# Performance work log

Hardware: AMD Instinct MI355X
Metric: run time of the kernel (lower is better)

Reference implementation:

```python
import jax, jax.numpy as jnp
import numpy as np

B, S, H, NH = 8, 1024, 1024, 16
HD = H // NH  # 64


def _rope(x, cos, sin):
    # x: [B, NH, S, HD]; cos/sin: [1, 1, S, HD]
    x1, x2 = jnp.split(x, 2, axis=-1)
    x_rot = jnp.concatenate((-x2, x1), axis=-1)
    return x * cos + x_rot * sin


def setup_inputs() -> dict:
    key = jax.random.key(0)
    ks = jax.random.split(key, 12)
    std = 1.0 / np.sqrt(H)
    inp = {
        "hidden_states": jax.random.normal(ks[0], (B, S, H), dtype=jnp.float32),
        "cos": jax.random.uniform(ks[1], (S, HD), dtype=jnp.float32),
        "sin": jax.random.uniform(ks[2], (S, HD), dtype=jnp.float32),
        "Wq": jax.random.normal(ks[3], (H, H), dtype=jnp.float32) * std,
        "bq": jnp.zeros((H,), dtype=jnp.float32),
        "Wk": jax.random.normal(ks[4], (H, H), dtype=jnp.float32) * std,
        "bk": jnp.zeros((H,), dtype=jnp.float32),
        "Wv": jax.random.normal(ks[5], (H, H), dtype=jnp.float32) * std,
        "bv": jnp.zeros((H,), dtype=jnp.float32),
        "Wo": jax.random.normal(ks[6], (H, H), dtype=jnp.float32) * std,
        "bo": jnp.zeros((H,), dtype=jnp.float32),
    }
    return inp


def reference(hidden_states, cos, sin, Wq, bq, Wk, bk, Wv, bv, Wo, bo):
    def split_heads(t):  # [B,S,H] -> [B,NH,S,HD]
        return t.reshape(B, S, NH, HD).transpose(0, 2, 1, 3)

    q = split_heads(hidden_states @ Wq.T + bq)
    k = split_heads(hidden_states @ Wk.T + bk)
    v = split_heads(hidden_states @ Wv.T + bv)

    c = cos.reshape(1, 1, S, HD)
    s = sin.reshape(1, 1, S, HD)
    q = _rope(q, c, s)
    k = _rope(k, c, s)

    scale = 1.0 / jnp.sqrt(jnp.asarray(HD, dtype=q.dtype))
    scores = jnp.einsum("bhqd,bhkd->bhqk", q, k) * scale
    attn = jax.nn.softmax(scores, axis=-1)
    out = jnp.einsum("bhqk,bhkd->bhqd", attn, v)  # [B,NH,S,HD]
    out = out.transpose(0, 2, 1, 3).reshape(B, S, H)
    return out @ Wo.T + bo
```

## Files before the change

kernel.cpp:

```cpp
#include <hip/hip_runtime.h>
#include <hip/hip_bf16.h>
#include <stdint.h>


typedef __bf16 bf16_t;
typedef __bf16 bf16x8 __attribute__((ext_vector_type(8)));
typedef __bf16 bf16x4 __attribute__((ext_vector_type(4)));
typedef float  f32x4  __attribute__((ext_vector_type(4)));
typedef float  f32x16 __attribute__((ext_vector_type(16)));
typedef uint32_t u32x4 __attribute__((ext_vector_type(4)));
typedef uint32_t u32x2 __attribute__((ext_vector_type(2)));

typedef __attribute__((address_space(1))) const void* as1_cvp;
typedef __attribute__((address_space(3))) void* as3_vp;

__device__ __forceinline__ f32x4 mfma16(bf16x8 a, bf16x8 b, f32x4 c) {
  return __builtin_amdgcn_mfma_f32_16x16x32_bf16(a, b, c, 0, 0, 0);
}
__device__ __forceinline__ f32x16 mfma32(bf16x8 a, bf16x8 b, f32x16 c) {
  return __builtin_amdgcn_mfma_f32_32x32x16_bf16(a, b, c, 0, 0, 0);
}

__device__ __forceinline__ void gload_lds16(const bf16_t* g, bf16_t* l) {
  __builtin_amdgcn_global_load_lds((as1_cvp)g, (as3_vp)l, 16, 0, 0);
}

__device__ __forceinline__ f32x4 zero4() {
  f32x4 z = {0.f, 0.f, 0.f, 0.f};
  return z;
}

__device__ __forceinline__ uint32_t pk2(float a, float b) {
  union { bf16_t h[2]; uint32_t u; } x;
  x.h[0] = (bf16_t)a;
  x.h[1] = (bf16_t)b;
  return x.u;
}

__global__ void cvt_all(const float* __restrict__ hs, const float* __restrict__ wq,
                        const float* __restrict__ wk, const float* __restrict__ wv,
                        const float* __restrict__ wo, bf16_t* __restrict__ Xb,
                        bf16_t* __restrict__ Wqkvb, bf16_t* __restrict__ Wob) {
  const int i = blockIdx.x * 256 + threadIdx.x;
  const f32x4* src;
  bf16x4* dst;
  if (i < 2097152) {
    src = (const f32x4*)hs + i;            dst = (bf16x4*)Xb + i;
  } else if (i < 2359296) {
    src = (const f32x4*)wq + (i - 2097152); dst = (bf16x4*)Wqkvb + (i - 2097152);
  } else if (i < 2621440) {
    src = (const f32x4*)wk + (i - 2359296); dst = (bf16x4*)Wqkvb + (i - 2359296) + 262144;
  } else if (i < 2883584) {
    src = (const f32x4*)wv + (i - 2621440); dst = (bf16x4*)Wqkvb + (i - 2621440) + 524288;
  } else {
    src = (const f32x4*)wo + (i - 2883584); dst = (bf16x4*)Wob + (i - 2883584);
  }
  const f32x4 v = *src;
  bf16x4 o;
  o[0] = (bf16_t)v[0]; o[1] = (bf16_t)v[1];
  o[2] = (bf16_t)v[2]; o[3] = (bf16_t)v[3];
  *dst = o;
}

template <int MODE>
__global__ __launch_bounds__(256, 3) void gemm128(
    const bf16_t* __restrict__ A, const bf16_t* __restrict__ Bw,
    const float* __restrict__ bQ, const float* __restrict__ bK,
    const float* __restrict__ bV, const float* __restrict__ cosp,
    const float* __restrict__ sinp,
    bf16_t* __restrict__ Qb, bf16_t* __restrict__ Kb, bf16_t* __restrict__ Vtb,
    float* __restrict__ Cout) {
  __shared__ bf16_t sm[128 * 64 * 2];
  bf16_t* sA = sm;
  bf16_t* sB = sm + 128 * 64;

  const int tid = threadIdx.x;
  const int lane = tid & 63;
  const int wid = tid >> 6;
  const int l15 = lane & 15;
  const int l4 = lane >> 4;
  const int row0 = blockIdx.x * 128;
  const int col0 = blockIdx.y * 128;
  const int wr = (wid >> 1) * 64;
  const int wc = (wid & 1) * 64;

  f32x4 acc[4][4];
#pragma unroll
  for (int mi = 0; mi < 4; ++mi)
#pragma unroll
    for (int ni = 0; ni < 4; ++ni) acc[mi][ni] = zero4();

  for (int kt = 0; kt < 16; ++kt) {
    const int k0 = kt * 64;
#pragma unroll
    for (int i = 0; i < 4; ++i) {
      const int chunk = i * 256 + tid;
      const int r = chunk >> 3, cc = chunk & 7;
      const int scc = cc ^ (r & 7);
      gload_lds16(A + (size_t)(row0 + r) * 1024 + k0 + scc * 8,
                  sA + (i * 256 + wid * 64) * 8);
      gload_lds16(Bw + (size_t)(col0 + r) * 1024 + k0 + scc * 8,
                  sB + (i * 256 + wid * 64) * 8);
    }
    __syncthreads();
    __builtin_amdgcn_s_setprio(1);
#pragma unroll
    for (int ks = 0; ks < 2; ++ks) {
      bf16x8 af[4], bfv[4];
#pragma unroll
      for (int mi = 0; mi < 4; ++mi) {
        const int r = wr + mi * 16 + l15;
        af[mi] = *(const bf16x8*)(sA + r * 64 + (((ks * 4 + l4) ^ (r & 7)) << 3));
      }
#pragma unroll
      for (int ni = 0; ni < 4; ++ni) {
        const int r = wc + ni * 16 + l15;
        bfv[ni] = *(const bf16x8*)(sB + r * 64 + (((ks * 4 + l4) ^ (r & 7)) << 3));
      }
#pragma unroll
      for (int mi = 0; mi < 4; ++mi)
#pragma unroll
        for (int ni = 0; ni < 4; ++ni)
          acc[mi][ni] = mfma16(af[mi], bfv[ni], acc[mi][ni]);
    }
    __builtin_amdgcn_s_setprio(0);
    __syncthreads();
  }

  if constexpr (MODE == 0) {
    const int proj = blockIdx.y >> 3;
    const float* bias = proj == 0 ? bQ : (proj == 1 ? bK : bV);
    if (proj < 2) {
      bf16_t* dst = proj == 0 ? Qb : Kb;
      const float qs = proj == 0 ? 0.18033688011112042f : 1.0f;
      const int base = col0 & 1023;
#pragma unroll
      for (int mi = 0; mi < 4; ++mi)
#pragma unroll
        for (int nl = 0; nl < 2; ++nl) {
          const int gcL = base + wc + nl * 16 + l15;
          const int h = gcL >> 6, dL = gcL & 63;
          const float bbL = bias[gcL], bbH = bias[gcL + 32];
#pragma unroll
          for (int j = 0; j < 4; ++j) {
            const int gr = row0 + wr + mi * 16 + l4 * 4 + j;
            const int b = gr >> 10, s = gr & 1023;
            const float cL = cosp[s * 64 + dL], cH = cosp[s * 64 + dL + 32];
            const float snL = sinp[s * 64 + dL], snH = sinp[s * 64 + dL + 32];
            const float x1 = acc[mi][nl][j] + bbL;
            const float x2 = acc[mi][nl + 2][j] + bbH;
            bf16_t* p = dst + ((size_t)(b * 16 + h) * 1024 + s) * 64 + dL;
            p[0]  = (bf16_t)((x1 * cL - x2 * snL) * qs);
            p[32] = (bf16_t)((x2 * cH + x1 * snH) * qs);
          }
        }
    } else {
      bf16_t* trb = sm;
#pragma unroll
      for (int mi = 0; mi < 4; ++mi)
#pragma unroll
        for (int ni = 0; ni < 4; ++ni) {
          const int cl = wc + ni * 16 + l15;
          const float bb = bias[(col0 & 1023) + cl];
#pragma unroll
          for (int j = 0; j < 4; ++j) {
            const int rl = wr + mi * 16 + l4 * 4 + j;
            trb[cl * 128 + (((rl >> 3) ^ (cl & 7)) << 3) + (rl & 7)] =
                (bf16_t)(acc[mi][ni][j] + bb);
          }
        }
      __syncthreads();
      const int b = row0 >> 10, s0 = row0 & 1023;
#pragma unroll
      for (int i = 0; i < 8; ++i) {
        const int chunk = i * 256 + tid;
        const int cl = chunk >> 4, rc = chunk & 15;
        const u32x4 v = *(const u32x4*)(trb + cl * 128 + ((rc ^ (cl & 7)) << 3));
        const int cv = (col0 & 1023) + cl;
        *(u32x4*)(Vtb + ((size_t)(b * 16 + (cv >> 6)) * 64 + (cv & 63)) * 1024 +
                  s0 + rc * 8) = v;
      }
    }
  } else {
#pragma unroll
    for (int mi = 0; mi < 4; ++mi)
#pragma unroll
      for (int ni = 0; ni < 4; ++ni) {
        const int gc = col0 + wc + ni * 16 + l15;
        const float bb = bQ[gc];
#pragma unroll
        for (int j = 0; j < 4; ++j) {
          const int gr = row0 + wr + mi * 16 + l4 * 4 + j;
          Cout[(size_t)gr * 1024 + gc] = acc[mi][ni][j] + bb;
        }
      }
  }
}

__global__ __launch_bounds__(256, 2) void attn_kernel(
    const bf16_t* __restrict__ Qb, const bf16_t* __restrict__ Kb,
    const bf16_t* __restrict__ Vtb, bf16_t* __restrict__ AOb) {
  __shared__ bf16_t sm[16384];
  bf16_t* sK = sm;
  bf16_t* sV = sm + 4096;
  const int tid = threadIdx.x, lane = tid & 63, wid = tid >> 6;
  const int l31 = lane & 31, l5 = lane >> 5;
  const bool loh = (l5 == 0);
  (void)loh;

  const int bh = blockIdx.x;
  const int q0 = blockIdx.y * 256;
  const bf16_t* Qg = Qb + (size_t)bh * 65536;
  const bf16_t* Kg = Kb + (size_t)bh * 65536;
  const bf16_t* Vg = Vtb + (size_t)bh * 65536;

#pragma unroll
  for (int i = 0; i < 8; ++i) {
    const int chunk = i * 256 + tid, r = chunk >> 3, c = chunk & 7;
    *(u32x4*)(sm + r * 64 + ((c ^ (r & 7)) << 3)) =
        *(const u32x4*)(Qg + (size_t)(q0 + r) * 64 + c * 8);
  }
  __syncthreads();
  bf16x8 qf[2][4];
#pragma unroll
  for (int qb = 0; qb < 2; ++qb)
#pragma unroll
    for (int step = 0; step < 4; ++step) {
      const int r = wid * 64 + qb * 32 + l31;
      qf[qb][step] =
          *(const bf16x8*)(sm + r * 64 + (((step * 2 + l5) ^ (r & 7)) << 3));
    }
  __syncthreads();

  const int ck1 = 256 + tid;
  const int kr0 = tid >> 3, kc0 = tid & 7;
  const int kr1 = ck1 >> 3, kc1 = ck1 & 7;
  bf16_t* kd0 = sK + kr0 * 64 + ((kc0 ^ (kr0 & 7)) << 3);
  bf16_t* kd1 = sK + kr1 * 64 + ((kc1 ^ (kr1 & 7)) << 3);
  bf16_t* vd0 = sV + kr0 * 64 + ((kc0 ^ (kr0 & 7)) << 3);
  bf16_t* vd1 = sV + kr1 * 64 + ((kc1 ^ (kr1 & 7)) << 3);
  const bf16_t* ksrc0 = Kg + kr0 * 64 + kc0 * 8;
  const bf16_t* ksrc1 = Kg + kr1 * 64 + kc1 * 8;
  const bf16_t* vsrc0 = Vg + kr0 * 1024 + kc0 * 8;
  const bf16_t* vsrc1 = Vg + kr1 * 1024 + kc1 * 8;

  u32x4 kv0 = *(const u32x4*)ksrc0;
  u32x4 kv1 = *(const u32x4*)ksrc1;
  u32x4 kv2 = *(const u32x4*)vsrc0;
  u32x4 kv3 = *(const u32x4*)vsrc1;

  f32x16 accO[2][2];
#pragma unroll
  for (int qb = 0; qb < 2; ++qb)
#pragma unroll
    for (int db = 0; db < 2; ++db)
#pragma unroll
      for (int r = 0; r < 16; ++r) accO[qb][db][r] = 0.f;
  float l_p[2] = {0.f, 0.f};

  for (int kt = 0; kt < 16; ++kt) {
    *(u32x4*)kd0 = kv0;
    *(u32x4*)kd1 = kv1;
    *(u32x4*)vd0 = kv2;
    *(u32x4*)vd1 = kv3;
    __syncthreads();
    if (kt < 15) {
      kv0 = *(const u32x4*)(ksrc0 + (kt + 1) * 4096);
      kv1 = *(const u32x4*)(ksrc1 + (kt + 1) * 4096);
      kv2 = *(const u32x4*)(vsrc0 + (kt + 1) * 64);
      kv3 = *(const u32x4*)(vsrc1 + (kt + 1) * 64);
    }

#pragma unroll
    for (int kb = 0; kb < 2; ++kb) {
      bf16x8 kf[4];
#pragma unroll
      for (int step = 0; step < 4; ++step) {
        const int r = kb * 32 + l31;
        kf[step] =
            *(const bf16x8*)(sK + r * 64 + (((step * 2 + l5) ^ (r & 7)) << 3));
      }
      f32x16 st0, st1;
#pragma unroll
      for (int r = 0; r < 16; ++r) { st0[r] = 0.f; st1[r] = 0.f; }
      __builtin_amdgcn_s_setprio(1);
#pragma unroll
      for (int step = 0; step < 4; ++step)
        st0 = mfma32(kf[step], qf[0][step], st0);
#pragma unroll
      for (int step = 0; step < 4; ++step)
        st1 = mfma32(kf[step], qf[1][step], st1);
      __builtin_amdgcn_s_setprio(0);

      float p0[16], p1[16];
      float rsa = 0.f, rsb = 0.f, rsc = 0.f, rsd = 0.f;
#pragma unroll
      for (int r = 0; r < 16; r += 2) {
        p0[r] = __builtin_amdgcn_exp2f(st0[r]);
        p0[r + 1] = __builtin_amdgcn_exp2f(st0[r + 1]);
        rsa += p0[r];
        rsb += p0[r + 1];
        p1[r] = __builtin_amdgcn_exp2f(st1[r]);
        p1[r + 1] = __builtin_amdgcn_exp2f(st1[r + 1]);
        rsc += p1[r];
        rsd += p1[r + 1];
      }
      l_p[0] += rsa + rsb;
      l_p[1] += rsc + rsd;

#pragma unroll
      for (int cb = 0; cb < 2; ++cb) {
        const int c = kb * 2 + cb;
        bf16x8 vf[2];
#pragma unroll
        for (int db = 0; db < 2; ++db) {
          const int d = db * 32 + l31;
          vf[db] =
              *(const bf16x8*)(sV + d * 64 + (((c * 2 + l5) ^ (d & 7)) << 3));
        }

        const uint32_t A0q0 = pk2(p0[8 * cb + 0], p0[8 * cb + 1]);
        const uint32_t B0q0 = pk2(p0[8 * cb + 2], p0[8 * cb + 3]);
        const uint32_t A1q0 = pk2(p0[8 * cb + 4], p0[8 * cb + 5]);
        const uint32_t B1q0 = pk2(p0[8 * cb + 6], p0[8 * cb + 7]);
        const uint32_t A0q1 = pk2(p1[8 * cb + 0], p1[8 * cb + 1]);
        const uint32_t B0q1 = pk2(p1[8 * cb + 2], p1[8 * cb + 3]);
        const uint32_t A1q1 = pk2(p1[8 * cb + 4], p1[8 * cb + 5]);
        const uint32_t B1q1 = pk2(p1[8 * cb + 6], p1[8 * cb + 7]);

        u32x4 w0, w1;
#if __has_builtin(__builtin_amdgcn_permlane32_swap)
        {
          const u32x2 ra0 = __builtin_amdgcn_permlane32_swap(A0q0, A1q0, false, false);
          const u32x2 rb0 = __builtin_amdgcn_permlane32_swap(B0q0, B1q0, false, false);
          w0[0] = ra0.x; w0[1] = rb0.x; w0[2] = ra0.y; w0[3] = rb0.y;
          const u32x2 ra1 = __builtin_amdgcn_permlane32_swap(A0q1, A1q1, false, false);
          const u32x2 rb1 = __builtin_amdgcn_permlane32_swap(B0q1, B1q1, false, false);
          w1[0] = ra1.x; w1[1] = rb1.x; w1[2] = ra1.y; w1[3] = rb1.y;
        }
#else
        {
          const uint32_t TAq0 = __shfl_xor(loh ? A1q0 : A0q0, 32);
          const uint32_t TBq0 = __shfl_xor(loh ? B1q0 : B0q0, 32);
          w0[0] = loh ? A0q0 : TAq0;
          w0[1] = loh ? B0q0 : TBq0;
          w0[2] = loh ? TAq0 : A1q0;
          w0[3] = loh ? TBq0 : B1q0;
          const uint32_t TAq1 = __shfl_xor(loh ? A1q1 : A0q1, 32);
          const uint32_t TBq1 = __shfl_xor(loh ? B1q1 : B0q1, 32);
          w1[0] = loh ? A0q1 : TAq1;
          w1[1] = loh ? B0q1 : TBq1;
          w1[2] = loh ? TAq1 : A1q1;
          w1[3] = loh ? TBq1 : B1q1;
        }
#endif
        const bf16x8 pa0 = __builtin_bit_cast(bf16x8, w0);
        const bf16x8 pa1 = __builtin_bit_cast(bf16x8, w1);

        __builtin_amdgcn_s_setprio(1);
        accO[0][0] = mfma32(vf[0], pa0, accO[0][0]);
        accO[0][1] = mfma32(vf[1], pa0, accO[0][1]);
        accO[1][0] = mfma32(vf[0], pa1, accO[1][0]);
        accO[1][1] = mfma32(vf[1], pa1, accO[1][1]);
        __builtin_amdgcn_s_setprio(0);
      }
    }
    __syncthreads();
  }

  float li[2];
#pragma unroll
  for (int qb = 0; qb < 2; ++qb) {
    const float t = l_p[qb] + __shfl_xor(l_p[qb], 32);
    li[qb] = __builtin_amdgcn_rcpf(t);
  }

  const int b = bh >> 4, h = bh & 15;
#pragma unroll
  for (int qb = 0; qb < 2; ++qb) {
    const int s = q0 + wid * 64 + qb * 32 + l31;
    bf16_t* rowp = AOb + ((size_t)b * 1024 + s) * 1024 + h * 64;
#pragma unroll
    for (int db = 0; db < 2; ++db)
#pragma unroll
      for (int g = 0; g < 4; ++g) {
        bf16x4 o;
#pragma unroll
        for (int j = 0; j < 4; ++j)
          o[j] = (bf16_t)(accO[qb][db][g * 4 + j] * li[qb]);
        *(bf16x4*)(rowp + db * 32 + g * 8 + l5 * 4) = o;
      }
  }
}

extern "C" void kernel_launch(void* const* d_in, const int* in_sizes, int n_in,
                              void* d_out, int out_size, void* d_ws,
                              size_t ws_size, hipStream_t stream) {
  const float* hs = (const float*)d_in[0];
  const float* cs = (const float*)d_in[1];
  const float* sn = (const float*)d_in[2];
  const float* Wq = (const float*)d_in[3];
  const float* bq = (const float*)d_in[4];
  const float* Wk = (const float*)d_in[5];
  const float* bk = (const float*)d_in[6];
  const float* Wv = (const float*)d_in[7];
  const float* bv = (const float*)d_in[8];
  const float* Wo = (const float*)d_in[9];
  const float* bo = (const float*)d_in[10];
  float* out = (float*)d_out;

  char* ws = (char*)d_ws;
  bf16_t* Xb    = (bf16_t*)(ws + 0);
  bf16_t* Wqkvb = (bf16_t*)(ws + 16777216);
  bf16_t* Wob   = (bf16_t*)(ws + 23068672);
  bf16_t* Qb    = (bf16_t*)(ws + 25165824);
  bf16_t* Kb    = (bf16_t*)(ws + 41943040);
  bf16_t* Vtb   = (bf16_t*)(ws + 58720256);
  bf16_t* AOb   = (bf16_t*)(ws + 75497472);

  cvt_all<<<12288, 256, 0, stream>>>(hs, Wq, Wk, Wv, Wo, Xb, Wqkvb, Wob);
  gemm128<0><<<dim3(64, 24), 256, 0, stream>>>(Xb, Wqkvb, bq, bk, bv, cs, sn,
                                               Qb, Kb, Vtb, nullptr);
  attn_kernel<<<dim3(128, 4), 256, 0, stream>>>(Qb, Kb, Vtb, AOb);
  gemm128<1><<<dim3(64, 8), 256, 0, stream>>>(AOb, Wob, bo, nullptr, nullptr,
                                              nullptr, nullptr, nullptr,
                                              nullptr, nullptr, out);
}
```

Before: 134.1 us.

## Double-buffer 128-key K/V tiles in LDS via direct global-to-LDS loads

Replaces the register-staged K/V prefetch (global load to registers, then LDS store, one 64-key tile per barrier) with global_load_lds direct copies into a double-buffered LDS region holding 128-key tiles. Q is also loaded straight into LDS. The aim is to halve the number of outer iterations and barriers, remove the VGPR staging, and overlap the next tile's load with compute. LDS use doubles to 64KB, which may limit occupancy at 2 blocks per CU. The visible part of the loop shows no barrier or waitcnt before the loads overwrite the alternate buffer, so correctness depends on code not shown.

After: 177.2 us. 32.2% more time.

```diff
diff --git a/kernel.cpp b/kernel.cpp
--- a/kernel.cpp
+++ b/kernel.cpp
@@ -200,9 +200,7 @@
 __global__ __launch_bounds__(256, 2) void attn_kernel(
     const bf16_t* __restrict__ Qb, const bf16_t* __restrict__ Kb,
     const bf16_t* __restrict__ Vtb, bf16_t* __restrict__ AOb) {
-  __shared__ bf16_t sm[16384];
-  bf16_t* sK = sm;
-  bf16_t* sV = sm + 4096;
+  __shared__ bf16_t sm[32768];
   const int tid = threadIdx.x, lane = tid & 63, wid = tid >> 6;
   const int l31 = lane & 31, l5 = lane >> 5;
   const bool loh = (l5 == 0);
@@ -214,13 +212,24 @@
   const bf16_t* Kg = Kb + (size_t)bh * 65536;
   const bf16_t* Vg = Vtb + (size_t)bh * 65536;
 
-#pragma unroll
-  for (int i = 0; i < 8; ++i) {
-    const int chunk = i * 256 + tid, r = chunk >> 3, c = chunk & 7;
-    *(u32x4*)(sm + r * 64 + ((c ^ (r & 7)) << 3)) =
-        *(const u32x4*)(Qg + (size_t)(q0 + r) * 64 + c * 8);
-  }
+  const int rr = tid >> 3, sc = (tid & 7) ^ (rr & 7);
+  const int dv = tid >> 4, sv = (tid & 15) ^ (dv & 7);
+  const bf16_t* Qsrc = Qg + (size_t)(q0 + rr) * 64 + sc * 8;
+  const bf16_t* Ksrc = Kg + (size_t)rr * 64 + sc * 8;
+  const bf16_t* Vsrc = Vg + (size_t)dv * 1024 + sv * 8;
+  const int dstw = wid * 512;
+
+#pragma unroll
+  for (int i = 0; i < 8; ++i)
+    gload_lds16(Qsrc + (size_t)i * 2048, sm + i * 2048 + dstw);
+#pragma unroll
+  for (int i = 0; i < 4; ++i)
+    gload_lds16(Ksrc + (size_t)i * 2048, sm + 16384 + i * 2048 + dstw);
+#pragma unroll
+  for (int i = 0; i < 4; ++i)
+    gload_lds16(Vsrc + (size_t)i * 16384, sm + 24576 + i * 2048 + dstw);
   __syncthreads();
+
   bf16x8 qf[2][4];
 #pragma unroll
   for (int qb = 0; qb < 2; ++qb)
@@ -232,23 +241,6 @@
     }
   __syncthreads();
 
-  const int ck1 = 256 + tid;
-  const int kr0 = tid >> 3, kc0 = tid & 7;
-  const int kr1 = ck1 >> 3, kc1 = ck1 & 7;
-  bf16_t* kd0 = sK + kr0 * 64 + ((kc0 ^ (kr0 & 7)) << 3);
-  bf16_t* kd1 = sK + kr1 * 64 + ((kc1 ^ (kr1 & 7)) << 3);
-  bf16_t* vd0 = sV + kr0 * 64 + ((kc0 ^ (kr0 & 7)) << 3);
-  bf16_t* vd1 = sV + kr1 * 64 + ((kc1 ^ (kr1 & 7)) << 3);
-  const bf16_t* ksrc0 = Kg + kr0 * 64 + kc0 * 8;
-  const bf16_t* ksrc1 = Kg + kr1 * 64 + kc1 * 8;
-  const bf16_t* vsrc0 = Vg + kr0 * 1024 + kc0 * 8;
-  const bf16_t* vsrc1 = Vg + kr1 * 1024 + kc1 * 8;
-
-  u32x4 kv0 = *(const u32x4*)ksrc0;
-  u32x4 kv1 = *(const u32x4*)ksrc1;
-  u32x4 kv2 = *(const u32x4*)vsrc0;
-  u32x4 kv3 = *(const u32x4*)vsrc1;
-
   f32x16 accO[2][2];
 #pragma unroll
   for (int qb = 0; qb < 2; ++qb)
@@ -258,31 +250,32 @@
       for (int r = 0; r < 16; ++r) accO[qb][db][r] = 0.f;
   float l_p[2] = {0.f, 0.f};
 
-  for (int kt = 0; kt < 16; ++kt) {
-    *(u32x4*)kd0 = kv0;
-    *(u32x4*)kd1 = kv1;
-    *(u32x4*)vd0 = kv2;
-    *(u32x4*)vd1 = kv3;
-    __syncthreads();
-    if (kt < 15) {
-      kv0 = *(const u32x4*)(ksrc0 + (kt + 1) * 4096);
-      kv1 = *(const u32x4*)(ksrc1 + (kt + 1) * 4096);
-      kv2 = *(const u32x4*)(vsrc0 + (kt + 1) * 64);
-      kv3 = *(const u32x4*)(vsrc1 + (kt + 1) * 64);
-    }
-
-#pragma unroll
-    for (int kb = 0; kb < 2; ++kb) {
+  for (int t = 0; t < 8; ++t) {
+    bf16_t* cb = sm + (((t + 1) & 1) << 14);
+    if (t < 7) {
+      bf16_t* nb = sm + ((t & 1) << 14);
+      const size_t kk = (size_t)(t + 1) * 128;
+#pragma unroll
+      for (int i = 0; i < 4; ++i)
+        gload_lds16(Ksrc + kk * 64 + (size_t)i * 2048, nb + i * 2048 + dstw);
+#pragma unroll
+      for (int i = 0; i < 4; ++i)
+        gload_lds16(Vsrc + kk + (size_t)i * 16384, nb + 8192 + i * 2048 + dstw);
+    }
+    bf16_t* sK = cb;
+    bf16_t* sV = cb + 8192;
+
+#pragma unroll
+    for (int kb = 0; kb < 4; ++kb) {
       bf16x8 kf[4];
-#pragma unroll
-      for (int step = 0; step < 4; ++step) {
-        const int r = kb * 32 + l31;
+      const int r = kb * 32 + l31;
+#pragma unroll
+      for (int step = 0; step < 4; ++step)
         kf[step] =
             *(const bf16x8*)(sK + r * 64 + (((step * 2 + l5) ^ (r & 7)) << 3));
-      }
       f32x16 st0, st1;
 #pragma unroll
-      for (int r = 0; r < 16; ++r) { st0[r] = 0.f; st1[r] = 0.f; }
+      for (int q = 0; q < 16; ++q) { st0[q] = 0.f; st1[q] = 0.f; }
       __builtin_amdgcn_s_setprio(1);
 #pragma unroll
       for (int step = 0; step < 4; ++step)
@@ -295,38 +288,38 @@
       float p0[16], p1[16];
       float rsa = 0.f, rsb = 0.f, rsc = 0.f, rsd = 0.f;
 #pragma unroll
-      for (int r = 0; r < 16; r += 2) {
-        p0[r] = __builtin_amdgcn_exp2f(st0[r]);
-        p0[r + 1] = __builtin_amdgcn_exp2f(st0[r + 1]);
-        rsa += p0[r];
-        rsb += p0[r + 1];
-        p1[r] = __builtin_amdgcn_exp2f(st1[r]);
-        p1[r + 1] = __builtin_amdgcn_exp2f(st1[r + 1]);
-        rsc += p1[r];
-        rsd += p1[r + 1];
+      for (int q = 0; q < 16; q += 2) {
+        p0[q] = __builtin_amdgcn_exp2f(st0[q]);
+        p0[q + 1] = __builtin_amdgcn_exp2f(st0[q + 1]);
+        rsa += p0[q];
+        rsb += p0[q + 1];
+        p1[q] = __builtin_amdgcn_exp2f(st1[q]);
+        p1[q + 1] = __builtin_amdgcn_exp2f(st1[q + 1]);
+        rsc += p1[q];
+        rsd += p1[q + 1];
       }
       l_p[0] += rsa + rsb;
       l_p[1] += rsc + rsd;
 
 #pragma unroll
-      for (int cb = 0; cb < 2; ++cb) {
-        const int c = kb * 2 + cb;
+      for (int cbk = 0; cbk < 2; ++cbk) {
+        const int c = kb * 2 + cbk;
         bf16x8 vf[2];
 #pragma unroll
         for (int db = 0; db < 2; ++db) {
           const int d = db * 32 + l31;
           vf[db] =
-              *(const bf16x8*)(sV + d * 64 + (((c * 2 + l5) ^ (d & 7)) << 3));
-        }
-
-        const uint32_t A0q0 = pk2(p0[8 * cb + 0], p0[8 * cb + 1]);
-        const uint32_t B0q0 = pk2(p0[8 * cb + 2], p0[8 * cb + 3]);
-        const uint32_t A1q0 = pk2(p0[8 * cb + 4], p0[8 * cb + 5]);
-        const uint32_t B1q0 = pk2(p0[8 * cb + 6], p0[8 * cb + 7]);
-        const uint32_t A0q1 = pk2(p1[8 * cb + 0], p1[8 * cb + 1]);
-        const uint32_t B0q1 = pk2(p1[8 * cb + 2], p1[8 * cb + 3]);
-        const uint32_t A1q1 = pk2(p1[8 * cb + 4], p1[8 * cb + 5]);
-        const uint32_t B1q1 = pk2(p1[8 * cb + 6], p1[8 * cb + 7]);
+              *(const bf16x8*)(sV + d * 128 + (((c * 2 + l5) ^ (d & 7)) << 3));
+        }
+
+        const uint32_t A0q0 = pk2(p0[8 * cbk + 0], p0[8 * cbk + 1]);
+        const uint32_t B0q0 = pk2(p0[8 * cbk + 2], p0[8 * cbk + 3]);
+        const uint32_t A1q0 = pk2(p0[8 * cbk + 4], p0[8 * cbk + 5]);
+        const uint32_t B1q0 = pk2(p0[8 * cbk + 6], p0[8 * cbk + 7]);
+        const uint32_t A0q1 = pk2(p1[8 * cbk + 0], p1[8 * cbk + 1]);
+        const uint32_t B0q1 = pk2(p1[8 * cbk + 2], p1[8 * cbk + 3]);
+        const uint32_t A1q1 = pk2(p1[8 * cbk + 4], p1[8 * cbk + 5]);
+        const uint32_t B1q1 = pk2(p1[8 * cbk + 6], p1[8 * cbk + 7]);
 
         u32x4 w0, w1;
 #if __has_builtin(__builtin_amdgcn_permlane32_swap)
```
